# Kernel tuning notes

Measured on AMD Instinct MI355X. Metric: run time of the kernel, lower is better.

The kernel has to match this reference:

```python
import jax, jax.numpy as jnp
import numpy as np

D_MODEL = 2048
N_HEADS = 16
N_KV_HEADS = 4
D_K = D_MODEL // N_HEADS  # 128
N_REP = N_HEADS // N_KV_HEADS
WINDOW = 128  # current_window_size default
RMS_EPS = 1e-8
ROPE_BASE = 10000.0
MASK_FILL = -10000.0


def _rmsnorm(x, w):
    rms = jnp.sqrt(jnp.mean(x * x, axis=-1, keepdims=True) + RMS_EPS)
    return x / rms * w


def _rope(x, cos, sin):
    # x: [B, S, H, d_k]; cos/sin: [S, d_k//2]; pairs are interleaved (..., -1, 2)
    B, S, H, dk = x.shape
    xr = x.reshape(B, S, H, dk // 2, 2)
    x1, x2 = xr[..., 0], xr[..., 1]
    c = cos[None, :, None, :]
    s = sin[None, :, None, :]
    o1 = x1 * c - x2 * s
    o2 = x1 * s + x2 * c
    return jnp.stack([o1, o2], axis=-1).reshape(B, S, H, dk)


def setup_inputs() -> dict:
    key = jax.random.key(0)
    ks = jax.random.split(key, 10)
    B, S = 2, 2048
    std = 1.0 / np.sqrt(D_MODEL)
    inp = {
        "x": jax.random.normal(ks[0], (B, S, D_MODEL), dtype=jnp.float32),
        "Wq": jax.random.normal(ks[1], (D_MODEL, D_MODEL), dtype=jnp.float32) * std,
        "bq": jnp.zeros((D_MODEL,), dtype=jnp.float32),
        "Wk": jax.random.normal(ks[2], (N_KV_HEADS * D_K, D_MODEL), dtype=jnp.float32) * std,
        "bk": jnp.zeros((N_KV_HEADS * D_K,), dtype=jnp.float32),
        "Wv": jax.random.normal(ks[3], (N_KV_HEADS * D_K, D_MODEL), dtype=jnp.float32) * std,
        "bv": jnp.zeros((N_KV_HEADS * D_K,), dtype=jnp.float32),
        "Wo": jax.random.normal(ks[4], (D_MODEL, D_MODEL), dtype=jnp.float32) * std,
        "bo": jnp.zeros((D_MODEL,), dtype=jnp.float32),
        "qn_w": jnp.ones((D_K,), dtype=jnp.float32),
        "kn_w": jnp.ones((D_K,), dtype=jnp.float32),
        "scale": jnp.asarray(1.0 / np.sqrt(D_K), dtype=jnp.float32),
    }
    return inp


def reference(x, Wq, bq, Wk, bk, Wv, bv, Wo, bo, qn_w, kn_w, scale):
    B, S, D = x.shape
    # projections
    q = (x @ Wq.T + bq).reshape(B, S, N_HEADS, D_K)
    k = (x @ Wk.T + bk).reshape(B, S, N_KV_HEADS, D_K)
    v = (x @ Wv.T + bv).reshape(B, S, N_KV_HEADS, D_K)
    # per-head RMSNorm
    q = _rmsnorm(q, qn_w)
    k = _rmsnorm(k, kn_w)
    # RoPE
    inv_freq = 1.0 / (ROPE_BASE ** (jnp.arange(0, D_K, 2, dtype=jnp.float32) / D_K))
    t = jnp.arange(S, dtype=jnp.float32)
    freqs = t[:, None] * inv_freq[None, :]  # [S, D_K//2]
    cos, sin = jnp.cos(freqs), jnp.sin(freqs)
    q = _rope(q, cos, sin)
    k = _rope(k, cos, sin)
    # [B, H, S, d_k]
    q = q.transpose(0, 2, 1, 3)
    k = k.transpose(0, 2, 1, 3)
    v = v.transpose(0, 2, 1, 3)
    # GQA repeat (repeat_interleave on head dim)
    k = jnp.repeat(k, N_REP, axis=1)
    v = jnp.repeat(v, N_REP, axis=1)
    # dense sliding-window path (window < seq_len)
    scores = jnp.einsum("bhqd,bhkd->bhqk", q, k) * scale
    idx = jnp.arange(S)
    causal = idx[:, None] < idx[None, :]  # triu diag=1
    local = jnp.abs(idx[:, None] - idx[None, :]) > (WINDOW // 2)
    mask = causal | local
    scores = jnp.where(mask[None, None, :, :], MASK_FILL, scores)
    attn = jax.nn.softmax(scores, axis=-1)
    out = jnp.einsum("bhqk,bhkd->bhqd", attn, v)
    out = out.transpose(0, 2, 1, 3).reshape(B, S, D)
    return out @ Wo.T + bo
```

## Files before the change

### kernel.cpp

```cpp
#include <hip/hip_runtime.h>

#define BATCH 2
#define SEQ 2048
#define DMODEL 2048
#define NHEADS 16
#define NKV 4
#define DK 128
#define WINH 64
#define NQKV 3072

typedef unsigned short ushort_t;
typedef __attribute__((ext_vector_type(8))) __bf16 bf16x8;
typedef __attribute__((ext_vector_type(4))) float f32x4;

__device__ __forceinline__ float b2f(ushort_t u) {
    union { unsigned int i; float f; } v; v.i = ((unsigned int)u) << 16; return v.f;
}
__device__ __forceinline__ ushort_t f2b(float f) {
    union { float f; unsigned int i; } v; v.f = f;
    unsigned int r = v.i + 0x7FFFu + ((v.i >> 16) & 1u);
    return (ushort_t)(r >> 16);
}

__device__ __forceinline__ void gload_lds16(const ushort_t* g, ushort_t* l) {
    __builtin_amdgcn_global_load_lds(
        (__attribute__((address_space(1))) void*)(void*)const_cast<ushort_t*>(g),
        (__attribute__((address_space(3))) void*)l, 16, 0, 0);
}

__global__ __launch_bounds__(256) void prep(
    const float* __restrict__ x,  const float* __restrict__ Wq,
    const float* __restrict__ Wk, const float* __restrict__ Wv,
    const float* __restrict__ Wo, const float* __restrict__ bq,
    const float* __restrict__ bk, const float* __restrict__ bv,
    ushort_t* __restrict__ xb, ushort_t* __restrict__ wdst,
    float* __restrict__ bqkv, float2* __restrict__ rtab)
{
    const int blk = blockIdx.x;
    const int tid = threadIdx.x;
    if (blk < 4096) {
        int i = blk * 256 + tid;
        float4 a = *((const float4*)x + i * 2);
        float4 b = *((const float4*)x + i * 2 + 1);
        ushort_t o[8] = { f2b(a.x), f2b(a.y), f2b(a.z), f2b(a.w),
                          f2b(b.x), f2b(b.y), f2b(b.z), f2b(b.w) };
        *((uint4*)xb + i) = *(const uint4*)o;
    } else if (blk < 9216) {
        int i = (blk - 4096) * 256 + tid;
        int row = i >> 8, c8 = i & 255;
        const float* src;
        if      (row < 2048) src = Wq + (size_t)row * 2048;
        else if (row < 2560) src = Wk + (size_t)(row - 2048) * 2048;
        else if (row < 3072) src = Wv + (size_t)(row - 2560) * 2048;
        else                 src = Wo + (size_t)(row - 3072) * 2048;
        float4 a = *((const float4*)src + c8 * 2);
        float4 b = *((const float4*)src + c8 * 2 + 1);
        ushort_t o[8] = { f2b(a.x), f2b(a.y), f2b(a.z), f2b(a.w),
                          f2b(b.x), f2b(b.y), f2b(b.z), f2b(b.w) };
        *((uint4*)wdst + i) = *(const uint4*)o;
    } else if (blk < 9228) {
        int i = (blk - 9216) * 256 + tid;
        if (i < 2048) bqkv[i] = bq[i];
        else if (i < 2560) bqkv[i] = bk[i - 2048];
        else if (i < 3072) bqkv[i] = bv[i - 2560];
    } else {
        int i = (blk - 9228) * 256 + tid;
        int s = i >> 6, dd = i & 63;
        float invfreq = exp2f(-(float)(2 * dd) * (13.287712379549449f / 128.0f));
        float ang = (float)s * invfreq;
        rtab[i] = make_float2(cosf(ang), sinf(ang));
    }
}

__global__ __launch_bounds__(256) void gemm_qkv(
    const ushort_t* __restrict__ A, const ushort_t* __restrict__ W,
    const float* __restrict__ bias, ushort_t* __restrict__ C,
    int M, int N, int K)
{
    __shared__ __attribute__((aligned(16))) ushort_t sA[8192];
    __shared__ __attribute__((aligned(16))) ushort_t sB[8192];

    const int tid  = threadIdx.x;
    const int lane = tid & 63;
    const int wave = tid >> 6;
    const int nbn  = N >> 7;

    int nwg = gridDim.x;
    int bid = blockIdx.x;
    int nb  = (nwg & 7) ? bid : ((bid & 7) * (nwg >> 3) + (bid >> 3));
    const int bm = nb / nbn;
    const int bn = nb % nbn;
    const int m0 = bm << 7, n0 = bn << 7;
    const int wm = wave >> 1, wn = wave & 1;

    f32x4 acc[4][4] = {};

    const int frow = lane & 15;
    const int kg   = lane >> 4;

    const ushort_t* gA[4]; const ushort_t* gB[4];
    ushort_t* lA[4]; ushort_t* lB[4];
#pragma unroll
    for (int j = 0; j < 4; ++j) {
        int t = wave * 4 + j;
        int c = t * 64 + lane;
        int r = c >> 3, s = c & 7;
        int ksrc = s ^ (r & 7);
        gA[j] = A + (size_t)(m0 + r) * K + ksrc * 8;
        gB[j] = W + (size_t)(n0 + r) * K + ksrc * 8;
        lA[j] = sA + t * 512;
        lB[j] = sB + t * 512;
    }

    for (int k0 = 0; k0 < K; k0 += 64) {
        if (k0) __syncthreads();
#pragma unroll
        for (int j = 0; j < 4; ++j) gload_lds16(gA[j] + k0, lA[j]);
#pragma unroll
        for (int j = 0; j < 4; ++j) gload_lds16(gB[j] + k0, lB[j]);
        __syncthreads();

        bf16x8 af[4][2], bfr[4][2];
#pragma unroll
        for (int mi = 0; mi < 4; ++mi)
#pragma unroll
            for (int kk = 0; kk < 2; ++kk) {
                int r = (wm << 6) + (mi << 4) + frow;
                int sl = (kk * 4 + kg) ^ (r & 7);
                af[mi][kk] = *(const bf16x8*)(sA + (r * 8 + sl) * 8);
            }
#pragma unroll
        for (int ni = 0; ni < 4; ++ni)
#pragma unroll
            for (int kk = 0; kk < 2; ++kk) {
                int r = (wn << 6) + (ni << 4) + frow;
                int sl = (kk * 4 + kg) ^ (r & 7);
                bfr[ni][kk] = *(const bf16x8*)(sB + (r * 8 + sl) * 8);
            }
#pragma unroll
        for (int kk = 0; kk < 2; ++kk)
#pragma unroll
            for (int mi = 0; mi < 4; ++mi)
#pragma unroll
                for (int ni = 0; ni < 4; ++ni)
                    acc[mi][ni] = __builtin_amdgcn_mfma_f32_16x16x32_bf16(
                        af[mi][kk], bfr[ni][kk], acc[mi][ni], 0, 0, 0);
    }

    const int orow = (lane >> 4) << 2;
    const int ocol = lane & 15;
#pragma unroll
    for (int ni = 0; ni < 4; ++ni) {
        int col = n0 + (wn << 6) + (ni << 4) + ocol;
        float bvf = bias[col];
#pragma unroll
        for (int mi = 0; mi < 4; ++mi) {
#pragma unroll
            for (int r = 0; r < 4; ++r) {
                int row = m0 + (wm << 6) + (mi << 4) + orow + r;
                C[(size_t)row * N + col] = f2b(acc[mi][ni][r] + bvf);
            }
        }
    }
}

__global__ __launch_bounds__(512) void gemm_out_ks(
    const ushort_t* __restrict__ A, const ushort_t* __restrict__ W,
    const float* __restrict__ bias, float* __restrict__ C,
    int M, int N, int K)
{
    __shared__ __attribute__((aligned(16))) unsigned char smem[65536];
    float* red = (float*)smem;

    const int tid  = threadIdx.x;
    const int lane = tid & 63;
    const int wave = tid >> 6;
    const int g    = wave >> 2;
    const int q    = wave & 3;
    const int wm   = q >> 1, wn = q & 1;
    const int nbn  = N >> 7;

    int nwg = gridDim.x;
    int bid = blockIdx.x;
    int nb  = (nwg & 7) ? bid : ((bid & 7) * (nwg >> 3) + (bid >> 3));
    const int bm = nb / nbn;
    const int bn = nb % nbn;
    const int m0 = bm << 7, n0 = bn << 7;

    f32x4 acc[4][4] = {};

    const int frow = lane & 15;
    const int kg   = lane >> 4;

    const ushort_t* gA[2]; const ushort_t* gB[2];
    int eofs[2];
#pragma unroll
    for (int j = 0; j < 2; ++j) {
        int t = wave * 2 + j;
        int c = t * 64 + lane;
        int r = c >> 3, s = c & 7;
        int ksrc = s ^ (r & 7);
        gA[j] = A + (size_t)(m0 + r) * K + ksrc * 8;
        gB[j] = W + (size_t)(n0 + r) * K + ksrc * 8;
        eofs[j] = t * 512;
    }

    const int nt = K >> 6;
#pragma unroll
    for (int j = 0; j < 2; ++j) {
        gload_lds16(gA[j], (ushort_t*)smem + eofs[j]);
        gload_lds16(gB[j], (ushort_t*)(smem + 16384) + eofs[j]);
    }
    __syncthreads();

    for (int t = 0; t < nt; ++t) {
        const int cur = t & 1;
        if (t + 1 < nt) {
            const int nxt = cur ^ 1;
            const int ko = (t + 1) << 6;
#pragma unroll
            for (int j = 0; j < 2; ++j) {
                gload_lds16(gA[j] + ko, (ushort_t*)(smem + nxt * 32768) + eofs[j]);
                gload_lds16(gB[j] + ko, (ushort_t*)(smem + nxt * 32768 + 16384) + eofs[j]);
            }
        }
        const ushort_t* bufA = (const ushort_t*)(smem + cur * 32768);
        const ushort_t* bufB = (const ushort_t*)(smem + cur * 32768 + 16384);

        bf16x8 af[4], bfr[4];
#pragma unroll
        for (int mi = 0; mi < 4; ++mi) {
            int r = (wm << 6) + (mi << 4) + frow;
            int sl = ((g << 2) + kg) ^ (r & 7);
            af[mi] = *(const bf16x8*)(bufA + (r * 8 + sl) * 8);
        }
#pragma unroll
        for (int ni = 0; ni < 4; ++ni) {
            int r = (wn << 6) + (ni << 4) + frow;
            int sl = ((g << 2) + kg) ^ (r & 7);
            bfr[ni] = *(const bf16x8*)(bufB + (r * 8 + sl) * 8);
        }
#pragma unroll
        for (int mi = 0; mi < 4; ++mi)
#pragma unroll
            for (int ni = 0; ni < 4; ++ni)
                acc[mi][ni] = __builtin_amdgcn_mfma_f32_16x16x32_bf16(
                    af[mi], bfr[ni], acc[mi][ni], 0, 0, 0);

        __syncthreads();
    }

    if (g == 1) {
#pragma unroll
        for (int mi = 0; mi < 4; ++mi)
#pragma unroll
            for (int ni = 0; ni < 4; ++ni)
                *(f32x4*)(red + q * 4096 + (mi * 4 + ni) * 256 + lane * 4) =
                    acc[mi][ni];
    }
    __syncthreads();

    if (g == 0) {
        const int orow = (lane >> 4) << 2;
        const int ocol = lane & 15;
#pragma unroll
        for (int ni = 0; ni < 4; ++ni) {
            int col = n0 + (wn << 6) + (ni << 4) + ocol;
            float bvf = bias[col];
#pragma unroll
            for (int mi = 0; mi < 4; ++mi) {
                f32x4 other = *(const f32x4*)(red + q * 4096 + (mi * 4 + ni) * 256 + lane * 4);
#pragma unroll
                for (int r = 0; r < 4; ++r) {
                    int row = m0 + (wm << 6) + (mi << 4) + orow + r;
                    C[(size_t)row * N + col] = acc[mi][ni][r] + other[r] + bvf;
                }
            }
        }
    }
}

__global__ __launch_bounds__(256) void attn_mfma(
    const ushort_t* __restrict__ qkv, const float* __restrict__ qn_w,
    const float* __restrict__ kn_w, const float* __restrict__ scp,
    const float2* __restrict__ rtab, ushort_t* __restrict__ ao)
{
    __shared__ __attribute__((aligned(16))) ushort_t sK[16384];
    __shared__ __attribute__((aligned(16))) ushort_t sVT[16384];

    const int tid  = threadIdx.x;
    const int lane = tid & 63;
    const int w    = tid >> 6;
    const int c    = lane & 15;
    const int g    = lane >> 4;

    const int blk = blockIdx.x;
    const int qt  = blk & 31;
    const int h   = (blk >> 5) & 15;
    const int b   = blk >> 9;
    const int kvh = h >> 2;
    const int i0  = qt << 6;
    const int jb  = i0 - 64;
    const float scale = scp[0];

    bf16x8 aq[4];
    {
        const int srow = i0 + w * 16 + c;
        const ushort_t* qp = qkv + ((size_t)(b * 2048 + srow)) * NQKV
                                 + h * 128 + g * 8;
        float xv[4][8];
        float ss = 0.f;
#pragma unroll
        for (int ks = 0; ks < 4; ++ks) {
            ushort_t raw[8];
            *(uint4*)raw = *(const uint4*)(qp + ks * 32);
#pragma unroll
            for (int j = 0; j < 8; ++j) {
                float xf = b2f(raw[j]);
                xv[ks][j] = xf;
                ss += xf * xf;
            }
        }
        ss += __shfl_xor(ss, 16, 64);
        ss += __shfl_xor(ss, 32, 64);
        float inv = rsqrtf(ss * (1.0f / 128.0f) + 1e-8f) * scale;
#pragma unroll
        for (int ks = 0; ks < 4; ++ks) {
            ushort_t outb[8];
#pragma unroll
            for (int jj = 0; jj < 4; ++jj) {
                int d = ks * 32 + g * 8 + 2 * jj;
                float2 w2 = *(const float2*)(qn_w + d);
                float x0 = xv[ks][2 * jj]     * inv * w2.x;
                float x1 = xv[ks][2 * jj + 1] * inv * w2.y;
                float2 cs = rtab[(srow << 6) + (d >> 1)];
                outb[2 * jj]     = f2b(x0 * cs.x - x1 * cs.y);
                outb[2 * jj + 1] = f2b(x0 * cs.y + x1 * cs.x);
            }
            aq[ks] = *(const bf16x8*)outb;
        }
    }

    const ushort_t* kvb = qkv + ((size_t)b * 2048) * NQKV + 2048 + kvh * 128;
#pragma unroll
    for (int it = 0; it < 8; ++it) {
        int idx = it * 256 + tid;
        int rr = idx >> 4, cc = idx & 15;
        int j = jb + rr; if (j < 0) j = 0;
        ushort_t raw[8];
        *(uint4*)raw = *(const uint4*)(kvb + (size_t)j * NQKV + cc * 8);
        float xv[8];
        float ss = 0.f;
#pragma unroll
        for (int jj = 0; jj < 8; ++jj) {
            xv[jj] = b2f(raw[jj]);
            ss += xv[jj] * xv[jj];
        }
        ss += __shfl_xor(ss, 1, 64);
        ss += __shfl_xor(ss, 2, 64);
        ss += __shfl_xor(ss, 4, 64);
        ss += __shfl_xor(ss, 8, 64);
        float inv = rsqrtf(ss * (1.0f / 128.0f) + 1e-8f);
        ushort_t outb[8];
#pragma unroll
        for (int jj = 0; jj < 4; ++jj) {
            int d = cc * 8 + 2 * jj;
            float2 w2 = *(const float2*)(kn_w + d);
            float x0 = xv[2 * jj]     * inv * w2.x;
            float x1 = xv[2 * jj + 1] * inv * w2.y;
            float2 cs = rtab[(j << 6) + (d >> 1)];
            outb[2 * jj]     = f2b(x0 * cs.x - x1 * cs.y);
            outb[2 * jj + 1] = f2b(x0 * cs.y + x1 * cs.x);
        }
        int f2v = (rr & 15) ^ ((rr >> 3) & 15);
        *(uint4*)(sK + (rr * 16 + (cc ^ f2v)) * 8) = *(const uint4*)outb;
    }
#pragma unroll
    for (int it = 0; it < 4; ++it) {
        int task = it * 256 + tid;
        int pp = task >> 4, d8 = task & 15;
        int j0 = jb + 2 * pp;     if (j0 < 0) j0 = 0;
        int j1 = jb + 2 * pp + 1; if (j1 < 0) j1 = 0;
        ushort_t e0[8]; *(uint4*)e0 = *(const uint4*)(kvb + (size_t)j0 * NQKV + 512 + d8 * 8);
        ushort_t e1[8]; *(uint4*)e1 = *(const uint4*)(kvb + (size_t)j1 * NQKV + 512 + d8 * 8);
        int cc = pp >> 2;
#pragma unroll
        for (int jj = 0; jj < 8; ++jj) {
            int rr = d8 * 8 + jj;
            int f2v = (rr & 15) ^ ((rr >> 3) & 15);
            unsigned int word = (unsigned int)e0[jj] | ((unsigned int)e1[jj] << 16);
            *(unsigned int*)(sVT + (rr * 16 + (cc ^ f2v)) * 8 + (pp & 3) * 2) = word;
        }
    }
    __syncthreads();

    f32x4 s[8] = {};
#pragma unroll
    for (int nt = 0; nt < 8; ++nt) {
        int rr = nt * 16 + c;
        int f2v = (rr & 15) ^ ((rr >> 3) & 15);
#pragma unroll
        for (int ks = 0; ks < 4; ++ks) {
            bf16x8 bk = *(const bf16x8*)(sK + (rr * 16 + ((ks * 4 + g) ^ f2v)) * 8);
            s[nt] = __builtin_amdgcn_mfma_f32_16x16x32_bf16(aq[ks], bk, s[nt], 0, 0, 0);
        }
    }

    float linv[4];
#pragma unroll
    for (int r = 0; r < 4; ++r) {
        int qb = w * 16 + g * 4 + r;
#pragma unroll
        for (int nt = 0; nt < 8; ++nt) {
            int jl = nt * 16 + c;
            bool valid = (jl >= qb) && (jl <= qb + 64) && (i0 + jl >= 64);
            s[nt][r] = valid ? s[nt][r] : -1e30f;
        }
        float m = s[0][r];
#pragma unroll
        for (int nt = 1; nt < 8; ++nt) m = fmaxf(m, s[nt][r]);
#pragma unroll
        for (int off = 1; off <= 8; off <<= 1) m = fmaxf(m, __shfl_xor(m, off, 64));
        float sum = 0.f;
#pragma unroll
        for (int nt = 0; nt < 8; ++nt) {
            float e = __expf(s[nt][r] - m);
            s[nt][r] = e;
            sum += e;
        }
#pragma unroll
        for (int off = 1; off <= 8; off <<= 1) sum += __shfl_xor(sum, off, 64);
        linv[r] = 1.0f / sum;
    }

    __syncthreads();
    float* Pw = (float*)sK + w * 2048;
#pragma unroll
    for (int nt = 0; nt < 8; ++nt) {
#pragma unroll
        for (int r = 0; r < 4; ++r) {
            int q = g * 4 + r;
            int chunk = nt * 4 + (c >> 2);
            Pw[q * 128 + ((chunk ^ (q & 7)) * 4) + (c & 3)] = s[nt][r];
        }
    }

    f32x4 o[8] = {};
#pragma unroll
    for (int kt = 0; kt < 4; ++kt) {
        float pf[8];
#pragma unroll
        for (int e = 0; e < 2; ++e) {
            int chunk = kt * 8 + g * 2 + e;
            f32x4 v4 = *(const f32x4*)(Pw + c * 128 + ((chunk ^ (c & 7)) * 4));
            pf[e * 4 + 0] = v4[0]; pf[e * 4 + 1] = v4[1];
            pf[e * 4 + 2] = v4[2]; pf[e * 4 + 3] = v4[3];
        }
        ushort_t pb[8];
#pragma unroll
        for (int j = 0; j < 8; ++j) pb[j] = f2b(pf[j]);
        bf16x8 pa = *(const bf16x8*)pb;
#pragma unroll
        for (int dt = 0; dt < 8; ++dt) {
            int rr = dt * 16 + c;
            int f2v = (rr & 15) ^ ((rr >> 3) & 15);
            bf16x8 bv = *(const bf16x8*)(sVT + (rr * 16 + ((kt * 4 + g) ^ f2v)) * 8);
            o[dt] = __builtin_amdgcn_mfma_f32_16x16x32_bf16(pa, bv, o[dt], 0, 0, 0);
        }
    }

    const size_t orow0 = (size_t)(b * 2048 + i0 + w * 16);
#pragma unroll
    for (int dt = 0; dt < 8; ++dt) {
#pragma unroll
        for (int r = 0; r < 4; ++r) {
            int q = g * 4 + r;
            ao[(orow0 + q) * 2048 + h * 128 + dt * 16 + c] = f2b(o[dt][r] * linv[r]);
        }
    }
}

extern "C" void kernel_launch(void* const* d_in, const int* in_sizes, int n_in,
                              void* d_out, int out_size, void* d_ws, size_t ws_size,
                              hipStream_t stream)
{
    const float* x   = (const float*)d_in[0];
    const float* Wq  = (const float*)d_in[1];
    const float* bq  = (const float*)d_in[2];
    const float* Wk  = (const float*)d_in[3];
    const float* bk  = (const float*)d_in[4];
    const float* Wv  = (const float*)d_in[5];
    const float* bv  = (const float*)d_in[6];
    const float* Wo  = (const float*)d_in[7];
    const float* bo  = (const float*)d_in[8];
    const float* qnw = (const float*)d_in[9];
    const float* knw = (const float*)d_in[10];
    const float* scp = (const float*)d_in[11];
    float* out = (float*)d_out;

    const int M = BATCH * SEQ;
    ushort_t* xb    = (ushort_t*)d_ws;
    ushort_t* qkv0  = xb   + (size_t)M * DMODEL;
    ushort_t* Wqkvb = qkv0 + (size_t)M * NQKV;
    ushort_t* Wob   = Wqkvb + (size_t)NQKV * DMODEL;
    float*    bqkv  = (float*)(Wob + (size_t)DMODEL * DMODEL);
    float2*   rtab  = (float2*)(bqkv + 3072);
    ushort_t* ao    = xb;
    (void)ws_size; (void)in_sizes; (void)n_in; (void)out_size;

    prep<<<dim3(9740), 256, 0, stream>>>(x, Wq, Wk, Wv, Wo, bq, bk, bv,
                                         xb, Wqkvb, bqkv, rtab);
    gemm_qkv<<<dim3((M / 128) * (NQKV / 128)), 256, 0, stream>>>(
        xb, Wqkvb, bqkv, qkv0, M, NQKV, DMODEL);
    attn_mfma<<<dim3(BATCH * NHEADS * (SEQ / 64)), 256, 0, stream>>>(
        qkv0, qnw, knw, scp, rtab, ao);
    gemm_out_ks<<<dim3((M / 128) * (DMODEL / 128)), 512, 0, stream>>>(
        ao, Wob, bo, out, M, DMODEL, DMODEL);
}
```

Before: 138.3 us.

## Double-buffer QKV GEMM with larger 256x192 tiles and 512 threads

Rewrites the QKV projection GEMM to use 256x192 output tiles, 8 waves, and double-buffered LDS in dynamic shared memory. The next K-tile's global-to-LDS loads are issued before computing on the current one, with explicit vmcnt waits. The aim is to hide memory latency and raise data reuse per tile. In exchange, 112KB of LDS and 96 accumulator vectors per thread limit occupancy, and the grid shrinks to 256 workgroups.

```diff
diff --git a/kernel.cpp b/kernel.cpp
--- a/kernel.cpp
+++ b/kernel.cpp
@@ -72,93 +72,113 @@
     }
 }
 
-__global__ __launch_bounds__(256) void gemm_qkv(
+__global__ __launch_bounds__(512) void gemm_qkv_p(
     const ushort_t* __restrict__ A, const ushort_t* __restrict__ W,
     const float* __restrict__ bias, ushort_t* __restrict__ C,
     int M, int N, int K)
 {
-    __shared__ __attribute__((aligned(16))) ushort_t sA[8192];
-    __shared__ __attribute__((aligned(16))) ushort_t sB[8192];
+    extern __shared__ __attribute__((aligned(16))) ushort_t smem[];
 
     const int tid  = threadIdx.x;
     const int lane = tid & 63;
     const int wave = tid >> 6;
-    const int nbn  = N >> 7;
+    const int wm   = wave >> 2;
+    const int wn   = wave & 3;
+    const int nbn  = N / 192;
 
     int nwg = gridDim.x;
     int bid = blockIdx.x;
     int nb  = (nwg & 7) ? bid : ((bid & 7) * (nwg >> 3) + (bid >> 3));
     const int bm = nb / nbn;
     const int bn = nb % nbn;
-    const int m0 = bm << 7, n0 = bn << 7;
-    const int wm = wave >> 1, wn = wave & 1;
-
-    f32x4 acc[4][4] = {};
+    const int m0 = bm << 8;
+    const int n0 = bn * 192;
+
+    f32x4 acc[8][3] = {};
 
     const int frow = lane & 15;
     const int kg   = lane >> 4;
 
-    const ushort_t* gA[4]; const ushort_t* gB[4];
-    ushort_t* lA[4]; ushort_t* lB[4];
+    const ushort_t* gA[4]; const ushort_t* gB[3];
+    int aofs[4], bofs[3];
 #pragma unroll
     for (int j = 0; j < 4; ++j) {
-        int t = wave * 4 + j;
-        int c = t * 64 + lane;
+        int c = j * 512 + tid;
         int r = c >> 3, s = c & 7;
-        int ksrc = s ^ (r & 7);
-        gA[j] = A + (size_t)(m0 + r) * K + ksrc * 8;
-        gB[j] = W + (size_t)(n0 + r) * K + ksrc * 8;
-        lA[j] = sA + t * 512;
-        lB[j] = sB + t * 512;
-    }
-
-    for (int k0 = 0; k0 < K; k0 += 64) {
-        if (k0) __syncthreads();
-#pragma unroll
-        for (int j = 0; j < 4; ++j) gload_lds16(gA[j] + k0, lA[j]);
-#pragma unroll
-        for (int j = 0; j < 4; ++j) gload_lds16(gB[j] + k0, lB[j]);
-        __syncthreads();
-
-        bf16x8 af[4][2], bfr[4][2];
-#pragma unroll
-        for (int mi = 0; mi < 4; ++mi)
-#pragma unroll
-            for (int kk = 0; kk < 2; ++kk) {
-                int r = (wm << 6) + (mi << 4) + frow;
-                int sl = (kk * 4 + kg) ^ (r & 7);
-                af[mi][kk] = *(const bf16x8*)(sA + (r * 8 + sl) * 8);
-            }
-#pragma unroll
-        for (int ni = 0; ni < 4; ++ni)
-#pragma unroll
-            for (int kk = 0; kk < 2; ++kk) {
-                int r = (wn << 6) + (ni << 4) + frow;
-                int sl = (kk * 4 + kg) ^ (r & 7);
-                bfr[ni][kk] = *(const bf16x8*)(sB + (r * 8 + sl) * 8);
-            }
-#pragma unroll
-        for (int kk = 0; kk < 2; ++kk)
-#pragma unroll
-            for (int mi = 0; mi < 4; ++mi)
-#pragma unroll
-                for (int ni = 0; ni < 4; ++ni)
-                    acc[mi][ni] = __builtin_amdgcn_mfma_f32_16x16x32_bf16(
-                        af[mi][kk], bfr[ni][kk], acc[mi][ni], 0, 0, 0);
+        gA[j] = A + (size_t)(m0 + r) * K + (s ^ (r & 7)) * 8;
+        aofs[j] = (j * 512 + wave * 64) * 8;
+    }
+#pragma unroll
+    for (int j = 0; j < 3; ++j) {
+        int c = j * 512 + tid;
+        int r = c >> 3, s = c & 7;
+        gB[j] = W + (size_t)(n0 + r) * K + (s ^ (r & 7)) * 8;
+        bofs[j] = (j * 512 + wave * 64) * 8;
+    }
+
+    const int nt = K >> 6;
+#pragma unroll
+    for (int j = 0; j < 4; ++j) gload_lds16(gA[j], smem + aofs[j]);
+#pragma unroll
+    for (int j = 0; j < 3; ++j) gload_lds16(gB[j], smem + 32768 + bofs[j]);
+
+    for (int t = 0; t < nt; ++t) {
+        const int cur = t & 1;
+        if (t + 1 < nt) {
+            const int nxt = cur ^ 1;
+            const int ko = (t + 1) << 6;
+#pragma unroll
+            for (int j = 0; j < 4; ++j)
+                gload_lds16(gA[j] + ko, smem + nxt * 16384 + aofs[j]);
+#pragma unroll
+            for (int j = 0; j < 3; ++j)
+                gload_lds16(gB[j] + ko, smem + 32768 + nxt * 12288 + bofs[j]);
+            asm volatile("s_waitcnt vmcnt(7)" ::: "memory");
+        } else {
+            asm volatile("s_waitcnt vmcnt(0)" ::: "memory");
+        }
+        __builtin_amdgcn_s_barrier();
+        __builtin_amdgcn_sched_barrier(0);
+
+        const ushort_t* bufA = smem + cur * 16384;
+        const ushort_t* bufB = smem + 32768 + cur * 12288;
+#pragma unroll
+        for (int kk = 0; kk < 2; ++kk) {
+            bf16x8 af[8], bf[3];
+#pragma unroll
+            for (int mf = 0; mf < 8; ++mf) {
+                int r = wm * 128 + mf * 16 + frow;
+                af[mf] = *(const bf16x8*)(bufA + (r * 8 + ((kk * 4 + kg) ^ (r & 7))) * 8);
+            }
+#pragma unroll
+            for (int nf = 0; nf < 3; ++nf) {
+                int r = wn * 48 + nf * 16 + frow;
+                bf[nf] = *(const bf16x8*)(bufB + (r * 8 + ((kk * 4 + kg) ^ (r & 7))) * 8);
+            }
+#pragma unroll
+            for (int mf = 0; mf < 8; ++mf)
+#pragma unroll
+                for (int nf = 0; nf < 3; ++nf)
+                    acc[mf][nf] = __builtin_amdgcn_mfma_f32_16x16x32_bf16(
+                        af[mf], bf[nf], acc[mf][nf], 0, 0, 0);
+        }
+        asm volatile("s_waitcnt lgkmcnt(0)" ::: "memory");
+        __builtin_amdgcn_s_barrier();
+        __builtin_amdgcn_sched_barrier(0);
     }
 
     const int orow = (lane >> 4) << 2;
     const int ocol = lane & 15;
 #pragma unroll
-    for (int ni = 0; ni < 4; ++ni) {
-        int col = n0 + (wn << 6) + (ni << 4) + ocol;
+    for (int nf = 0; nf < 3; ++nf) {
+        int col = n0 + wn * 48 + nf * 16 + ocol;
         float bvf = bias[col];
 #pragma unroll
-        for (int mi = 0; mi < 4; ++mi) {
+        for (int mf = 0; mf < 8; ++mf) {
 #pragma unroll
             for (int r = 0; r < 4; ++r) {
-                int row = m0 + (wm << 6) + (mi << 4) + orow + r;
-                C[(size_t)row * N + col] = f2b(acc[mi][ni][r] + bvf);
+                int row = m0 + wm * 128 + mf * 16 + orow + r;
+                C[(size_t)row * N + col] = f2b(acc[mf][nf][r] + bvf);
             }
         }
     }
@@ -508,9 +528,12 @@
     ushort_t* ao    = xb;
     (void)ws_size; (void)in_sizes; (void)n_in; (void)out_size;
 
+    hipFuncSetAttribute((const void*)gemm_qkv_p,
+                        hipFuncAttributeMaxDynamicSharedMemorySize, 114688);
+
     prep<<<dim3(9740), 256, 0, stream>>>(x, Wq, Wk, Wv, Wo, bq, bk, bv,
                                          xb, Wqkvb, bqkv, rtab);
-    gemm_qkv<<<dim3((M / 128) * (NQKV / 128)), 256, 0, stream>>>(
+    gemm_qkv_p<<<dim3((M / 256) * (NQKV / 192)), 512, 114688, stream>>>(
         xb, Wqkvb, bqkv, qkv0, M, NQKV, DMODEL);
     attn_mfma<<<dim3(BATCH * NHEADS * (SEQ / 64)), 256, 0, stream>>>(
         qkv0, qnw, knw, scp, rtab, ao);
```

Result: no change. 136.3 us (-1.5%).

## Pipeline QKV GEMM with four-stage LDS ring and async prefetch

Applied to the files above, without the earlier changes.

Rewrites the QKV projection GEMM main loop so it runs over a 4-buffer LDS ring with a K-step of 32 and keeps three tiles of direct global-to-LDS loads in flight. Explicit vmcnt waits and a single barrier per step replace the two barriers per iteration, and s_setprio is raised around the MFMA block. The aim is to hide global memory latency behind the matrix math. In exchange it uses 64KB of LDS per block, which may limit occupancy, and it does more loop iterations with less MFMA work in each.

```diff
diff --git a/kernel.cpp b/kernel.cpp
--- a/kernel.cpp
+++ b/kernel.cpp
@@ -72,13 +72,12 @@
     }
 }
 
-__global__ __launch_bounds__(256) void gemm_qkv(
+__global__ __launch_bounds__(256) void gemm_qkv_q(
     const ushort_t* __restrict__ A, const ushort_t* __restrict__ W,
     const float* __restrict__ bias, ushort_t* __restrict__ C,
     int M, int N, int K)
 {
-    __shared__ __attribute__((aligned(16))) ushort_t sA[8192];
-    __shared__ __attribute__((aligned(16))) ushort_t sB[8192];
+    __shared__ __attribute__((aligned(16))) ushort_t smem[32768];
 
     const int tid  = threadIdx.x;
     const int lane = tid & 63;
@@ -98,53 +97,69 @@
     const int frow = lane & 15;
     const int kg   = lane >> 4;
 
-    const ushort_t* gA[4]; const ushort_t* gB[4];
-    ushort_t* lA[4]; ushort_t* lB[4];
-#pragma unroll
-    for (int j = 0; j < 4; ++j) {
-        int t = wave * 4 + j;
-        int c = t * 64 + lane;
-        int r = c >> 3, s = c & 7;
-        int ksrc = s ^ (r & 7);
-        gA[j] = A + (size_t)(m0 + r) * K + ksrc * 8;
-        gB[j] = W + (size_t)(n0 + r) * K + ksrc * 8;
-        lA[j] = sA + t * 512;
-        lB[j] = sB + t * 512;
-    }
-
-    for (int k0 = 0; k0 < K; k0 += 64) {
-        if (k0) __syncthreads();
-#pragma unroll
-        for (int j = 0; j < 4; ++j) gload_lds16(gA[j] + k0, lA[j]);
-#pragma unroll
-        for (int j = 0; j < 4; ++j) gload_lds16(gB[j] + k0, lB[j]);
-        __syncthreads();
-
-        bf16x8 af[4][2], bfr[4][2];
+    const ushort_t* gA[2]; const ushort_t* gB[2];
+    int ofs[2];
+#pragma unroll
+    for (int j = 0; j < 2; ++j) {
+        int c = j * 256 + tid;
+        int r = c >> 2, s = c & 3;
+        int ks = s ^ ((r >> 1) & 3);
+        gA[j] = A + (size_t)(m0 + r) * K + ks * 8;
+        gB[j] = W + (size_t)(n0 + r) * K + ks * 8;
+        ofs[j] = (j * 256 + wave * 64) * 8;
+    }
+
+    const int nt = K >> 5;
+#pragma unroll
+    for (int p = 0; p < 3; ++p) {
+        int ko = p << 5;
+        ushort_t* base = smem + p * 8192;
+        gload_lds16(gA[0] + ko, base + ofs[0]);
+        gload_lds16(gA[1] + ko, base + ofs[1]);
+        gload_lds16(gB[0] + ko, base + 4096 + ofs[0]);
+        gload_lds16(gB[1] + ko, base + 4096 + ofs[1]);
+    }
+
+    for (int t = 0; t < nt; ++t) {
+        if (t < nt - 2)       asm volatile("s_waitcnt vmcnt(8)" ::: "memory");
+        else if (t == nt - 2) asm volatile("s_waitcnt vmcnt(4)" ::: "memory");
+        else                  asm volatile("s_waitcnt vmcnt(0)" ::: "memory");
+        __builtin_amdgcn_s_barrier();
+        __builtin_amdgcn_sched_barrier(0);
+
+        if (t + 3 < nt) {
+            int ko = (t + 3) << 5;
+            ushort_t* base = smem + ((t + 3) & 3) * 8192;
+            gload_lds16(gA[0] + ko, base + ofs[0]);
+            gload_lds16(gA[1] + ko, base + ofs[1]);
+            gload_lds16(gB[0] + ko, base + 4096 + ofs[0]);
+            gload_lds16(gB[1] + ko, base + 4096 + ofs[1]);
+        }
+
+        const ushort_t* bufA = smem + (t & 3) * 8192;
+        const ushort_t* bufB = bufA + 4096;
+        bf16x8 af[4], bfr[4];
+#pragma unroll
+        for (int mi = 0; mi < 4; ++mi) {
+            int r = (wm << 6) + (mi << 4) + frow;
+            int sl = kg ^ ((r >> 1) & 3);
+            af[mi] = *(const bf16x8*)(bufA + (r * 4 + sl) * 8);
+        }
+#pragma unroll
+        for (int ni = 0; ni < 4; ++ni) {
+            int r = (wn << 6) + (ni << 4) + frow;
+            int sl = kg ^ ((r >> 1) & 3);
+            bfr[ni] = *(const bf16x8*)(bufB + (r * 4 + sl) * 8);
+        }
+        __builtin_amdgcn_s_setprio(1);
 #pragma unroll
         for (int mi = 0; mi < 4; ++mi)
 #pragma unroll
-            for (int kk = 0; kk < 2; ++kk) {
-                int r = (wm << 6) + (mi << 4) + frow;
-                int sl = (kk * 4 + kg) ^ (r & 7);
-                af[mi][kk] = *(const bf16x8*)(sA + (r * 8 + sl) * 8);
-            }
-#pragma unroll
-        for (int ni = 0; ni < 4; ++ni)
-#pragma unroll
-            for (int kk = 0; kk < 2; ++kk) {
-                int r = (wn << 6) + (ni << 4) + frow;
-                int sl = (kk * 4 + kg) ^ (r & 7);
-                bfr[ni][kk] = *(const bf16x8*)(sB + (r * 8 + sl) * 8);
-            }
-#pragma unroll
-        for (int kk = 0; kk < 2; ++kk)
-#pragma unroll
-            for (int mi = 0; mi < 4; ++mi)
-#pragma unroll
-                for (int ni = 0; ni < 4; ++ni)
-                    acc[mi][ni] = __builtin_amdgcn_mfma_f32_16x16x32_bf16(
-                        af[mi][kk], bfr[ni][kk], acc[mi][ni], 0, 0, 0);
+            for (int ni = 0; ni < 4; ++ni)
+                acc[mi][ni] = __builtin_amdgcn_mfma_f32_16x16x32_bf16(
+                    af[mi], bfr[ni], acc[mi][ni], 0, 0, 0);
+        __builtin_amdgcn_s_setprio(0);
+        asm volatile("s_waitcnt lgkmcnt(0)" ::: "memory");
     }
 
     const int orow = (lane >> 4) << 2;
@@ -510,7 +525,7 @@
 
     prep<<<dim3(9740), 256, 0, stream>>>(x, Wq, Wk, Wv, Wo, bq, bk, bv,
                                          xb, Wqkvb, bqkv, rtab);
-    gemm_qkv<<<dim3((M / 128) * (NQKV / 128)), 256, 0, stream>>>(
+    gemm_qkv_q<<<dim3((M / 128) * (NQKV / 128)), 256, 0, stream>>>(
         xb, Wqkvb, bqkv, qkv0, M, NQKV, DMODEL);
     attn_mfma<<<dim3(BATCH * NHEADS * (SEQ / 64)), 256, 0, stream>>>(
         qkv0, qnw, knw, scp, rtab, ao);
```

Result: slower. 147.6 us (+6.7%).
